# Kernel tuning notes

Measured on AMD Instinct MI355X. Metric: run time of the kernel, lower is better.

The kernel has to match this reference:

```python
import jax, jax.numpy as jnp
import numpy as np

B_COEF = 1.0  # b in __init__
F_POW = 1     # f in __init__
H_POW = 2     # h in __init__
N_NODES = 16384
DIM = 16


def setup_inputs() -> dict:
    key = jax.random.key(0)
    kA, kx = jax.random.split(key)
    # Adjacency with nonnegative entries (dense, as in the torch dense branch)
    A = jax.random.uniform(kA, (N_NODES, N_NODES), dtype=jnp.float32)
    x = jax.random.uniform(kx, (N_NODES, DIM), dtype=jnp.float32)
    return {"A": A, "x": x, "t": 0}


def reference(A, x, t):
    # dx/dt = -b * x^f + (A @ x^h) / (x^h + 1)
    # NOTE: python precedence in the original: (A @ x**h) / (x**h + 1)
    xh = x ** H_POW            # [n, dim]
    agg = A @ xh               # [n, dim] adjacency aggregation
    return -B_COEF * x ** F_POW + agg / (xh + 1.0)
```

## Files before the change

### kernel.cpp

```cpp
#include <hip/hip_runtime.h>
#include <stdint.h>


#define NN 16384
#define DIM 16
#define TPB 256
#define ROWS 32
#define NRB 512
#define KSPLIT 2
#define KRANGE 8192
#define KC 256
#define NCH 32

__global__ __launch_bounds__(256) void prep_kernel(const float* __restrict__ x,
                                                   float* __restrict__ out,
                                                   float* __restrict__ xh,
                                                   float* __restrict__ inv) {
    int i = blockIdx.x * 256 + threadIdx.x;
    float4 v = reinterpret_cast<const float4*>(x)[i];
    reinterpret_cast<float4*>(out)[i] = make_float4(-v.x, -v.y, -v.z, -v.w);
    float4 h = make_float4(v.x * v.x, v.y * v.y, v.z * v.z, v.w * v.w);
    reinterpret_cast<float4*>(xh)[i] = h;
    reinterpret_cast<float4*>(inv)[i] =
        make_float4(1.0f / (h.x + 1.0f), 1.0f / (h.y + 1.0f),
                    1.0f / (h.z + 1.0f), 1.0f / (h.w + 1.0f));
}

__device__ __forceinline__ void gload_lds16(const void* g, void* l, int nt) {
    if (nt)
        __builtin_amdgcn_global_load_lds(
            (const __attribute__((address_space(1))) void*)g,
            (__attribute__((address_space(3))) void*)l, 16, 0, 2 );
    else
        __builtin_amdgcn_global_load_lds(
            (const __attribute__((address_space(1))) void*)g,
            (__attribute__((address_space(3))) void*)l, 16, 0, 0);
}

__device__ __forceinline__ float4 shfl_xor4(float4 v, int mask) {
    return make_float4(__shfl_xor(v.x, mask), __shfl_xor(v.y, mask),
                       __shfl_xor(v.z, mask), __shfl_xor(v.w, mask));
}

__global__ __launch_bounds__(TPB)
__attribute__((amdgpu_waves_per_eu(1, 3)))
void agg_kernel(const float* __restrict__ A,
                const float* __restrict__ xh,
                const float* __restrict__ inv,
                float* __restrict__ out) {
    __shared__ float tA[ROWS * KC];
    __shared__ float tX[KC * DIM];

    const int tid = threadIdx.x;
    const int l = tid & 63, w = tid >> 6;
    const int m8 = l & 7, q8 = l >> 3;
    const int rb = blockIdx.x & (NRB - 1);
    const int ks = blockIdx.x >> 9;
    const int r0 = rb * ROWS;
    const size_t k0 = (size_t)ks * KRANGE;

    const float* Ab = A + (size_t)(r0 + 8 * w) * NN + k0;
    int aoff[8];
    #pragma unroll
    for (int i = 0; i < 8; ++i) aoff[i] = 4 * (l ^ (i & 7));

    const float* Xc = xh + k0 * DIM;
    int xoff[4];
    #pragma unroll
    for (int j = 0; j < 4; ++j) xoff[j] = (4 * w + j) * 256 + 4 * l;

    int rA[4][2];
    #pragma unroll
    for (int j = 0; j < 4; ++j)
        #pragma unroll
        for (int b = 0; b < 2; ++b)
            rA[j][b] = (m8 + 8 * j) * KC + 4 * ((16 * w + 2 * q8 + b) ^ m8);
    const int XBASE = (64 * w + 8 * q8) * 16;

    float4 acc[4][4];
    #pragma unroll
    for (int j = 0; j < 4; ++j)
        #pragma unroll
        for (int v = 0; v < 4; ++v) acc[j][v] = make_float4(0.f, 0.f, 0.f, 0.f);

    for (int t = 0; t < NCH; ++t) {
        __syncthreads();
        {
            const float* sA = Ab + (size_t)t * KC;
            #pragma unroll
            for (int i = 0; i < 8; ++i)
                gload_lds16(sA + (size_t)i * NN + aoff[i], &tA[(8 * w + i) * KC], 1);
            const float* sX = Xc + (size_t)t * (KC * DIM);
            #pragma unroll
            for (int j = 0; j < 4; ++j)
                gload_lds16(sX + xoff[j], &tX[(4 * w + j) * 256], 0);
        }
        __syncthreads();
        #pragma unroll
        for (int b = 0; b < 2; ++b) {
            float4 ar[4];
            #pragma unroll
            for (int j = 0; j < 4; ++j)
                ar[j] = *reinterpret_cast<const float4*>(&tA[rA[j][b]]);
            #pragma unroll
            for (int e = 0; e < 4; ++e) {
                const int xb = XBASE + (4 * b + e) * 16;
                float4 xv[4];
                #pragma unroll
                for (int v = 0; v < 4; ++v)
                    xv[v] = *reinterpret_cast<const float4*>(&tX[xb + 4 * v]);
                #pragma unroll
                for (int j = 0; j < 4; ++j) {
                    const float a = (&ar[j].x)[e];
                    #pragma unroll
                    for (int v = 0; v < 4; ++v) {
                        acc[j][v].x += a * xv[v].x;
                        acc[j][v].y += a * xv[v].y;
                        acc[j][v].z += a * xv[v].z;
                        acc[j][v].w += a * xv[v].w;
                    }
                }
            }
        }
    }

    {
        const int b2 = (q8 >> 2) & 1, b1 = (q8 >> 1) & 1, b0 = q8 & 1;
        #pragma unroll
        for (int j = 0; j < 2; ++j)
            #pragma unroll
            for (int v = 0; v < 4; ++v) {
                float4 send = b2 ? acc[j][v] : acc[j + 2][v];
                float4 keep = b2 ? acc[j + 2][v] : acc[j][v];
                float4 r = shfl_xor4(send, 32);
                acc[j][v] = make_float4(keep.x + r.x, keep.y + r.y,
                                        keep.z + r.z, keep.w + r.w);
            }
        #pragma unroll
        for (int v = 0; v < 4; ++v) {
            float4 send = b1 ? acc[0][v] : acc[1][v];
            float4 keep = b1 ? acc[1][v] : acc[0][v];
            float4 r = shfl_xor4(send, 16);
            acc[0][v] = make_float4(keep.x + r.x, keep.y + r.y,
                                    keep.z + r.z, keep.w + r.w);
        }
        #pragma unroll
        for (int v = 0; v < 2; ++v) {
            float4 send = b0 ? acc[0][v] : acc[0][v + 2];
            float4 keep = b0 ? acc[0][v + 2] : acc[0][v];
            float4 r = shfl_xor4(send, 8);
            acc[0][v] = make_float4(keep.x + r.x, keep.y + r.y,
                                    keep.z + r.z, keep.w + r.w);
        }
    }

    {
        const int R = r0 + m8 + 8 * (q8 >> 1);
        const int d0 = 8 * (q8 & 1);
        const float* ivp = inv + (size_t)R * DIM + d0;
        float* op = out + (size_t)R * DIM + d0;
        float4 iv0 = *reinterpret_cast<const float4*>(ivp);
        float4 iv1 = *reinterpret_cast<const float4*>(ivp + 4);
        atomicAdd(op + 0, acc[0][0].x * iv0.x);
        atomicAdd(op + 1, acc[0][0].y * iv0.y);
        atomicAdd(op + 2, acc[0][0].z * iv0.z);
        atomicAdd(op + 3, acc[0][0].w * iv0.w);
        atomicAdd(op + 4, acc[0][1].x * iv1.x);
        atomicAdd(op + 5, acc[0][1].y * iv1.y);
        atomicAdd(op + 6, acc[0][1].z * iv1.z);
        atomicAdd(op + 7, acc[0][1].w * iv1.w);
    }
}

extern "C" void kernel_launch(void* const* d_in, const int* in_sizes, int n_in,
                              void* d_out, int out_size, void* d_ws, size_t ws_size,
                              hipStream_t stream) {
    const float* A = (const float*)d_in[0];
    const float* x = (const float*)d_in[1];
    float* out = (float*)d_out;
    float* xhp = (float*)d_ws;
    float* inv = (float*)d_ws + (size_t)NN * DIM;

    prep_kernel<<<(NN * DIM / 4) / 256, 256, 0, stream>>>(x, out, xhp, inv);
    agg_kernel<<<NRB * KSPLIT, TPB, 0, stream>>>(A, xhp, inv, out);
}
```

Measured before the change: 240.8 us.

## Double-buffer LDS tiles and overlap global-to-LDS loads with compute

```diff
diff --git a/kernel.cpp b/kernel.cpp
--- a/kernel.cpp
+++ b/kernel.cpp
@@ -43,13 +43,13 @@
 }
 
 __global__ __launch_bounds__(TPB)
-__attribute__((amdgpu_waves_per_eu(1, 3)))
+__attribute__((amdgpu_waves_per_eu(1, 2)))
 void agg_kernel(const float* __restrict__ A,
                 const float* __restrict__ xh,
                 const float* __restrict__ inv,
                 float* __restrict__ out) {
-    __shared__ float tA[ROWS * KC];
-    __shared__ float tX[KC * DIM];
+    __shared__ float tA[2][ROWS * KC];
+    __shared__ float tX[2][KC * DIM];
 
     const int tid = threadIdx.x;
     const int l = tid & 63, w = tid >> 6;
@@ -83,46 +83,78 @@
         #pragma unroll
         for (int v = 0; v < 4; ++v) acc[j][v] = make_float4(0.f, 0.f, 0.f, 0.f);
 
-    for (int t = 0; t < NCH; ++t) {
-        __syncthreads();
-        {
-            const float* sA = Ab + (size_t)t * KC;
-            #pragma unroll
-            for (int i = 0; i < 8; ++i)
-                gload_lds16(sA + (size_t)i * NN + aoff[i], &tA[(8 * w + i) * KC], 1);
-            const float* sX = Xc + (size_t)t * (KC * DIM);
-            #pragma unroll
-            for (int j = 0; j < 4; ++j)
-                gload_lds16(sX + xoff[j], &tX[(4 * w + j) * 256], 0);
-        }
-        __syncthreads();
-        #pragma unroll
-        for (int b = 0; b < 2; ++b) {
-            float4 ar[4];
-            #pragma unroll
-            for (int j = 0; j < 4; ++j)
-                ar[j] = *reinterpret_cast<const float4*>(&tA[rA[j][b]]);
-            #pragma unroll
-            for (int e = 0; e < 4; ++e) {
-                const int xb = XBASE + (4 * b + e) * 16;
-                float4 xv[4];
-                #pragma unroll
-                for (int v = 0; v < 4; ++v)
-                    xv[v] = *reinterpret_cast<const float4*>(&tX[xb + 4 * v]);
-                #pragma unroll
-                for (int j = 0; j < 4; ++j) {
-                    const float a = (&ar[j].x)[e];
-                    #pragma unroll
-                    for (int v = 0; v < 4; ++v) {
-                        acc[j][v].x += a * xv[v].x;
-                        acc[j][v].y += a * xv[v].y;
-                        acc[j][v].z += a * xv[v].z;
-                        acc[j][v].w += a * xv[v].w;
-                    }
-                }
-            }
-        }
-    }
+#define STAGE(T, B)                                                           \
+    {                                                                         \
+        const float* sA = Ab + (size_t)(T) * KC;                              \
+        _Pragma("unroll")                                                     \
+        for (int i = 0; i < 8; ++i)                                           \
+            gload_lds16(sA + (size_t)i * NN + aoff[i],                        \
+                        &tA[B][(8 * w + i) * KC], 1);                         \
+        const float* sX = Xc + (size_t)(T) * (KC * DIM);                      \
+        _Pragma("unroll")                                                     \
+        for (int j = 0; j < 4; ++j)                                           \
+            gload_lds16(sX + xoff[j], &tX[B][(4 * w + j) * 256], 0);          \
+    }
+
+#define COMPUTE(B)                                                            \
+    {                                                                         \
+        _Pragma("unroll")                                                     \
+        for (int b = 0; b < 2; ++b) {                                         \
+            float4 ar[4];                                                     \
+            _Pragma("unroll")                                                 \
+            for (int j = 0; j < 4; ++j)                                       \
+                ar[j] = *reinterpret_cast<const float4*>(&tA[B][rA[j][b]]);   \
+            _Pragma("unroll")                                                 \
+            for (int e = 0; e < 4; ++e) {                                     \
+                const int xb = XBASE + (4 * b + e) * 16;                      \
+                float4 xv[4];                                                 \
+                _Pragma("unroll")                                             \
+                for (int v = 0; v < 4; ++v)                                   \
+                    xv[v] = *reinterpret_cast<const float4*>(&tX[B][xb + 4 * v]); \
+                _Pragma("unroll")                                             \
+                for (int j = 0; j < 4; ++j) {                                 \
+                    const float a = (&ar[j].x)[e];                            \
+                    _Pragma("unroll")                                         \
+                    for (int v = 0; v < 4; ++v) {                             \
+                        acc[j][v].x += a * xv[v].x;                           \
+                        acc[j][v].y += a * xv[v].y;                           \
+                        acc[j][v].z += a * xv[v].z;                           \
+                        acc[j][v].w += a * xv[v].w;                           \
+                    }                                                         \
+                }                                                             \
+            }                                                                 \
+        }                                                                     \
+    }
+
+#define WAIT_VM(N)                                                  \
+    asm volatile("s_waitcnt vmcnt(" #N ")" ::: "memory");           \
+    __builtin_amdgcn_sched_barrier(0);                              \
+    __builtin_amdgcn_s_barrier();
+
+#define WAIT_LGKM0                                                  \
+    asm volatile("s_waitcnt lgkmcnt(0)" ::: "memory");              \
+    __builtin_amdgcn_sched_barrier(0);                              \
+    __builtin_amdgcn_s_barrier();
+
+    STAGE(0, 0);
+
+    for (int tt = 0; tt < 15; ++tt) {
+        const int t0 = 2 * tt;
+        STAGE(t0 + 1, 1);
+        WAIT_VM(12)
+        COMPUTE(0)
+        WAIT_LGKM0
+        STAGE(t0 + 2, 0);
+        WAIT_VM(12)
+        COMPUTE(1)
+        WAIT_LGKM0
+    }
+    STAGE(31, 1);
+    WAIT_VM(12)
+    COMPUTE(0)
+    WAIT_LGKM0
+    WAIT_VM(0)
+    COMPUTE(1)
 
     {
         const int b2 = (q8 >> 2) & 1, b1 = (q8 >> 1) & 1, b0 = q8 & 1;
@@ -170,6 +202,10 @@
         atomicAdd(op + 6, acc[0][1].z * iv1.z);
         atomicAdd(op + 7, acc[0][1].w * iv1.w);
     }
+#undef STAGE
+#undef COMPUTE
+#undef WAIT_VM
+#undef WAIT_LGKM0
 }
 
 extern "C" void kernel_launch(void* const* d_in, const int* in_sizes, int n_in,
```

After: 369.0 us. 53.3% more time.
